# Kernel optimization log

Measured on AMD Instinct MI355X. Metric: run time of the kernel, lower is better.

The kernel has to match this reference:

```python
import jax, jax.numpy as jnp
import numpy as np

GATE_SLOPE = 10.0
ALPHA = 0.8
STRIDE = 1
PADDING = 1


def _unfold(x, kH, kW, stride, padding):
    # torch F.unfold equivalent, kept as (B, Cin, kH, kW, Hout, Wout)
    B, C, H, W = x.shape
    xp = jnp.pad(x, ((0, 0), (0, 0), (padding, padding), (padding, padding)))
    Hout = (H + 2 * padding - kH) // stride + 1
    Wout = (W + 2 * padding - kW) // stride + 1
    cols = []
    for i in range(kH):          # small fixed loop over kernel taps (9 iters)
        for j in range(kW):
            cols.append(xp[:, :, i:i + Hout * stride:stride, j:j + Wout * stride:stride])
    return jnp.stack(cols, axis=2).reshape(B, C, kH, kW, Hout, Wout)


def setup_inputs() -> dict:
    key = jax.random.key(0)
    ks = jax.random.split(key, 6)
    B, Cin, H, W = 4, 16, 32, 32
    Cout, K, kH, kW = 32, 3, 3, 3
    pshape = (Cout, Cin, K, kH, kW)
    x = jax.random.normal(ks[0], (B, Cin, H, W), jnp.float32)
    k = jax.random.uniform(ks[1], pshape, jnp.float32) * 2.0 + 0.5
    Ec = jax.random.uniform(ks[2], pshape, jnp.float32) * 2.0 + 0.5
    Ps = jax.random.uniform(ks[3], pshape, jnp.float32) * 1.5 + 0.5
    bias = jax.random.normal(ks[4], pshape, jnp.float32) * 0.1
    coef = jax.random.normal(ks[5], pshape, jnp.float32)
    out_bias = jnp.zeros((Cout,), jnp.float32)
    return {"x": x, "k": k, "Ec": Ec, "Ps": Ps, "bias": bias, "coef": coef, "out_bias": out_bias}


def reference(x, k, Ec, Ps, bias, coef, out_bias):
    kH, kW = k.shape[-2], k.shape[-1]
    patches = _unfold(x, kH, kW, STRIDE, PADDING)          # (B,Cin,kH,kW,Hout,Wout)
    # broadcast layout: (B, Cout, Cin, K, kH, kW, Hout, Wout)
    xe = patches[:, None, :, None]                          # (B,1,Cin,1,kH,kW,Ho,Wo)
    def bc(p):
        return p[None, :, :, :, :, :, None, None]
    k_, Ec_, Ps_, b_, c_ = bc(k), bc(Ec), bc(Ps), bc(bias), bc(coef)
    # stateless mode: prev_x = detach(x_exp) -> dx == 0 in value, grad flows via xe
    prev_x = jax.lax.stop_gradient(xe)
    is_moving_up = jax.nn.sigmoid(GATE_SLOPE * (xe - prev_x))
    crossed_pos = jax.nn.sigmoid(GATE_SLOPE * (xe - Ec_))
    crossed_neg = jax.nn.sigmoid(GATE_SLOPE * (-xe - Ec_))
    su = is_moving_up * crossed_pos
    sl = (1.0 - is_moving_up) * crossed_neg
    # branch_prev = +1 (stateless)
    target_sign = su - sl + (1.0 - su - sl)
    branch_mom = ALPHA + (1.0 - ALPHA) * target_sign
    shifted_x = xe + Ec_ * branch_mom
    basis = Ps_ * jnp.tanh(k_ * shifted_x) + b_
    out = jnp.sum(basis * c_, axis=(2, 3, 4, 5))            # (B,Cout,Hout,Wout)
    return out + out_bias[None, :, None, None]
```

## Files before the change

kernel.cpp:

```cpp
#include <hip/hip_runtime.h>


#define LOG2E 1.4426950408889634f

__global__ __launch_bounds__(256, 8) void ferro_main(
    const float* __restrict__ x,
    const float* __restrict__ k, const float* __restrict__ Ec,
    const float* __restrict__ Ps, const float* __restrict__ bias,
    const float* __restrict__ coef, const float* __restrict__ out_bias,
    float* __restrict__ out)
{
    const int bid = blockIdx.x;
    const int rs  = bid & 15;
    const int co  = (bid >> 4) & 31;
    const int b   = bid >> 9;
    const int tid = threadIdx.x;

    __shared__ float4 p4s[432];
    __shared__ float  xs[16 * 4 * 34];
    __shared__ float  red[128];
    __shared__ float  redc[4];
    __shared__ float  csh;

    const int pbase = co * 432;
    float cpart = 0.f;
    for (int s = tid; s < 432; s += 256) {
        float kv = k[pbase + s];
        float ev = Ec[pbase + s];
        float pv = Ps[pbase + s];
        float bv = bias[pbase + s];
        float cv = coef[pbase + s];
        float G  = 2.f * LOG2E * kv;
        float4 v;
        v.x = ev;
        v.y = G;
        v.z = 0.1f * G * ev;
        v.w = -2.f * pv * cv;
        int cin = s / 27;
        int r   = s - cin * 27;
        int kk  = r / 9;
        int ij  = r - kk * 9;
        p4s[cin * 27 + ij * 3 + kk] = v;
        cpart += (pv + bv) * cv;
    }

    const int r0 = rs * 2;
    const float* xb = x + b * (16 * 1024);
    for (int idx = tid; idx < 16 * 136; idx += 256) {
        int cin  = idx / 136;
        int rem  = idx - cin * 136;
        int row4 = rem / 34;
        int colp = rem - row4 * 34;
        int gr = r0 + row4 - 1;
        int gc = colp - 1;
        float v = 0.f;
        if ((unsigned)gr < 32u && (unsigned)gc < 32u)
            v = xb[(cin * 32 + gr) * 32 + gc];
        xs[idx] = v;
    }

    #pragma unroll
    for (int off = 32; off > 0; off >>= 1)
        cpart += __shfl_down(cpart, off, 64);
    if ((tid & 63) == 0) redc[tid >> 6] = cpart;
    __syncthreads();
    if (tid == 0) csh = redc[0] + redc[1] + redc[2] + redc[3];
    __syncthreads();

    const int lane = tid & 63;
    const int w    = tid >> 6;
    const int row  = w >> 1;
    const int cinq = w & 1;
    const int col  = lane & 31;
    const int cinh = lane >> 5;
    float acc0 = 0.f, acc1 = 0.f, acc2 = 0.f;

    const int cinbase = cinq * 8 + cinh * 4;
    #pragma unroll 1
    for (int c = 0; c < 4; ++c) {
        const int cin = cinbase + c;
        const float*  xr = &xs[cin * 136 + row * 34 + col];
        const float4* pp = &p4s[cin * 27];
        #pragma unroll
        for (int ij = 0; ij < 9; ++ij) {
            const int i = ij / 3, j = ij - (ij / 3) * 3;
            float xv = xr[i * 34 + j];
            {
                float4 v = pp[ij * 3 + 0];
                float wv = xv + v.x;
                float q  = fmaf(wv, wv, 0.04f);
                float r  = __builtin_amdgcn_rsqf(q);
                float t  = fmaf(wv, r, -1.f);
                float a  = fmaf(v.z, t, v.y * wv);
                float e  = __builtin_amdgcn_exp2f(a);
                float u  = __builtin_amdgcn_rcpf(e + 1.f);
                acc0 = fmaf(v.w, u, acc0);
            }
            {
                float4 v = pp[ij * 3 + 1];
                float wv = xv + v.x;
                float q  = fmaf(wv, wv, 0.04f);
                float r  = __builtin_amdgcn_rsqf(q);
                float t  = fmaf(wv, r, -1.f);
                float a  = fmaf(v.z, t, v.y * wv);
                float e  = __builtin_amdgcn_exp2f(a);
                float u  = __builtin_amdgcn_rcpf(e + 1.f);
                acc1 = fmaf(v.w, u, acc1);
            }
            {
                float4 v = pp[ij * 3 + 2];
                float wv = xv + v.x;
                float q  = fmaf(wv, wv, 0.04f);
                float r  = __builtin_amdgcn_rsqf(q);
                float t  = fmaf(wv, r, -1.f);
                float a  = fmaf(v.z, t, v.y * wv);
                float e  = __builtin_amdgcn_exp2f(a);
                float u  = __builtin_amdgcn_rcpf(e + 1.f);
                acc2 = fmaf(v.w, u, acc2);
            }
        }
    }

    float acc = (acc0 + acc1) + acc2;
    acc += __shfl_xor(acc, 32, 64);
    if (cinh == 0) red[w * 32 + col] = acc;
    __syncthreads();

    if (tid < 64) {
        int r   = tid >> 5;
        int cl  = tid & 31;
        float v = red[(r * 2 + 0) * 32 + cl] + red[(r * 2 + 1) * 32 + cl]
                + csh + out_bias[co];
        out[((b * 32 + co) * 32 + (r0 + r)) * 32 + cl] = v;
    }
}

extern "C" void kernel_launch(void* const* d_in, const int* in_sizes, int n_in,
                              void* d_out, int out_size, void* d_ws, size_t ws_size,
                              hipStream_t stream) {
    const float* x        = (const float*)d_in[0];
    const float* k        = (const float*)d_in[1];
    const float* Ec       = (const float*)d_in[2];
    const float* Ps       = (const float*)d_in[3];
    const float* bias     = (const float*)d_in[4];
    const float* coef     = (const float*)d_in[5];
    const float* out_bias = (const float*)d_in[6];
    float* out = (float*)d_out;

    ferro_main<<<dim3(2048), dim3(256), 0, stream>>>(
        x, k, Ec, Ps, bias, coef, out_bias, out);
}
```

Baseline: 87.69 us.

## Precompute per-channel parameter table in a prep kernel and read it wave-uniformly

Measured after the change: 89.42 us. About the same (+2.0%).

```diff
diff --git a/kernel.cpp b/kernel.cpp
--- a/kernel.cpp
+++ b/kernel.cpp
@@ -3,26 +3,19 @@
 
 #define LOG2E 1.4426950408889634f
 
-__global__ __launch_bounds__(256, 8) void ferro_main(
-    const float* __restrict__ x,
+#define WS_CONST_OFF (32 * 432)
+
+__global__ __launch_bounds__(256) void ferro_prep(
     const float* __restrict__ k, const float* __restrict__ Ec,
     const float* __restrict__ Ps, const float* __restrict__ bias,
-    const float* __restrict__ coef, const float* __restrict__ out_bias,
-    float* __restrict__ out)
+    const float* __restrict__ coef,
+    float4* __restrict__ wp, float* __restrict__ wc)
 {
-    const int bid = blockIdx.x;
-    const int rs  = bid & 15;
-    const int co  = (bid >> 4) & 31;
-    const int b   = bid >> 9;
+    const int co  = blockIdx.x;
     const int tid = threadIdx.x;
+    const int pbase = co * 432;
+    __shared__ float redc[4];
 
-    __shared__ float4 p4s[432];
-    __shared__ float  xs[16 * 4 * 34];
-    __shared__ float  red[128];
-    __shared__ float  redc[4];
-    __shared__ float  csh;
-
-    const int pbase = co * 432;
     float cpart = 0.f;
     for (int s = tid; s < 432; s += 256) {
         float kv = k[pbase + s];
@@ -40,9 +33,31 @@
         int r   = s - cin * 27;
         int kk  = r / 9;
         int ij  = r - kk * 9;
-        p4s[cin * 27 + ij * 3 + kk] = v;
+        wp[pbase + cin * 27 + ij * 3 + kk] = v;
         cpart += (pv + bv) * cv;
     }
+    #pragma unroll
+    for (int off = 32; off > 0; off >>= 1)
+        cpart += __shfl_down(cpart, off, 64);
+    if ((tid & 63) == 0) redc[tid >> 6] = cpart;
+    __syncthreads();
+    if (tid == 0) wc[co] = redc[0] + redc[1] + redc[2] + redc[3];
+}
+
+__global__ __launch_bounds__(256, 8) void ferro_main(
+    const float* __restrict__ x,
+    const float4* __restrict__ wp, const float* __restrict__ wc,
+    const float* __restrict__ out_bias,
+    float* __restrict__ out)
+{
+    const int bid = blockIdx.x;
+    const int rs  = bid & 15;
+    const int co  = (bid >> 4) & 31;
+    const int b   = bid >> 9;
+    const int tid = threadIdx.x;
+
+    __shared__ float xs[16 * 4 * 34];
+    __shared__ float red[4 * 64];
 
     const int r0 = rs * 2;
     const float* xb = x + b * (16 * 1024);
@@ -58,29 +73,20 @@
             v = xb[(cin * 32 + gr) * 32 + gc];
         xs[idx] = v;
     }
-
-    #pragma unroll
-    for (int off = 32; off > 0; off >>= 1)
-        cpart += __shfl_down(cpart, off, 64);
-    if ((tid & 63) == 0) redc[tid >> 6] = cpart;
-    __syncthreads();
-    if (tid == 0) csh = redc[0] + redc[1] + redc[2] + redc[3];
     __syncthreads();
 
     const int lane = tid & 63;
-    const int w    = tid >> 6;
-    const int row  = w >> 1;
-    const int cinq = w & 1;
+    const int wid  = __builtin_amdgcn_readfirstlane(tid >> 6);
+    const int row  = lane >> 5;
     const int col  = lane & 31;
-    const int cinh = lane >> 5;
+
     float acc0 = 0.f, acc1 = 0.f, acc2 = 0.f;
 
-    const int cinbase = cinq * 8 + cinh * 4;
     #pragma unroll 1
     for (int c = 0; c < 4; ++c) {
-        const int cin = cinbase + c;
+        const int cin = wid * 4 + c;
         const float*  xr = &xs[cin * 136 + row * 34 + col];
-        const float4* pp = &p4s[cin * 27];
+        const float4* pp = wp + (co * 432 + cin * 27);
         #pragma unroll
         for (int ij = 0; ij < 9; ++ij) {
             const int i = ij / 3, j = ij - (ij / 3) * 3;
@@ -121,17 +127,13 @@
         }
     }
 
-    float acc = (acc0 + acc1) + acc2;
-    acc += __shfl_xor(acc, 32, 64);
-    if (cinh == 0) red[w * 32 + col] = acc;
+    red[wid * 64 + lane] = (acc0 + acc1) + acc2;
     __syncthreads();
 
     if (tid < 64) {
-        int r   = tid >> 5;
-        int cl  = tid & 31;
-        float v = red[(r * 2 + 0) * 32 + cl] + red[(r * 2 + 1) * 32 + cl]
-                + csh + out_bias[co];
-        out[((b * 32 + co) * 32 + (r0 + r)) * 32 + cl] = v;
+        float v = red[tid] + red[64 + tid] + red[128 + tid] + red[192 + tid]
+                + wc[co] + out_bias[co];
+        out[((b * 32 + co) * 32 + (r0 + (tid >> 5))) * 32 + (tid & 31)] = v;
     }
 }
 
@@ -147,6 +149,9 @@
     const float* out_bias = (const float*)d_in[6];
     float* out = (float*)d_out;
 
-    ferro_main<<<dim3(2048), dim3(256), 0, stream>>>(
-        x, k, Ec, Ps, bias, coef, out_bias, out);
+    float4* wp = (float4*)d_ws;
+    float*  wc = (float*)d_ws + WS_CONST_OFF * 4;
+
+    ferro_prep<<<dim3(32), dim3(256), 0, stream>>>(k, Ec, Ps, bias, coef, wp, wc);
+    ferro_main<<<dim3(2048), dim3(256), 0, stream>>>(x, wp, wc, out_bias, out);
 }
```
